# Kernel tuning notes

Hardware: AMD Instinct MI355X
Metric: run time of the kernel (lower is better)

The kernel has to match this reference:

```python
import jax, jax.numpy as jnp
import numpy as np

B, N, CIN, H, E = 1, 20000, 128, 128, 320000


def setup_inputs() -> dict:
    key = jax.random.key(0)
    ks = jax.random.split(key, 16)
    x = jax.random.normal(ks[0], (B, N, CIN), jnp.float32)
    edge_index = jax.random.randint(ks[1], (2, E), 0, N, dtype=jnp.int64)
    edge_weight = jax.random.uniform(ks[2], (E,), jnp.float32)
    h = jax.random.normal(ks[3], (B, N, H), jnp.float32)
    c = jax.random.normal(ks[4], (B, N, H), jnp.float32)
    # GCN stack params, gate order [i, f, c, o]; 2 layers each (K=2)
    Wx0 = jax.random.normal(ks[5], (4, CIN, H), jnp.float32) / np.float32(np.sqrt(CIN))
    bx0 = jnp.zeros((4, H), jnp.float32)
    Wx1 = jax.random.normal(ks[6], (4, H, H), jnp.float32) / np.float32(np.sqrt(H))
    bx1 = jnp.zeros((4, H), jnp.float32)
    Wh0 = jax.random.normal(ks[7], (4, H, H), jnp.float32) / np.float32(np.sqrt(H))
    bh0 = jnp.zeros((4, H), jnp.float32)
    Wh1 = jax.random.normal(ks[8], (4, H, H), jnp.float32) / np.float32(np.sqrt(H))
    bh1 = jnp.zeros((4, H), jnp.float32)
    wc = jax.random.normal(ks[9], (3, H), jnp.float32) * 0.1  # peephole [i, f, o]
    bg = jnp.zeros((4, H), jnp.float32)  # gate biases [i, f, c, o]
    return dict(x=x, edge_index=edge_index, edge_weight=edge_weight, h=h, c=c,
                Wx0=Wx0, bx0=bx0, Wx1=Wx1, bx1=bx1,
                Wh0=Wh0, bh0=bh0, Wh1=Wh1, bh1=bh1, wc=wc, bg=bg)


def reference(x, edge_index, edge_weight, h, c,
              Wx0, bx0, Wx1, bx1, Wh0, bh0, Wh1, bh1, wc, bg):
    n = x.shape[1]
    src, dst = edge_index[0], edge_index[1]
    loop = jnp.arange(n)
    src2 = jnp.concatenate([src, loop])
    dst2 = jnp.concatenate([dst, loop])
    w2 = jnp.concatenate([edge_weight, jnp.ones((n,), edge_weight.dtype)])
    deg = jax.ops.segment_sum(w2, dst2, num_segments=n)
    dis = jnp.where(deg > 0, jax.lax.rsqrt(jnp.maximum(deg, 1e-12)), 0.0)
    norm = dis[src2] * w2 * dis[dst2]  # sym GCN norm with self loops

    def prop(t):  # t: [..., N, F] -> D^-1/2 (A+I) D^-1/2 t
        lead = t.shape[:-2]
        tf = t.reshape((-1,) + t.shape[-2:])
        m = tf[:, src2, :] * norm[None, :, None]
        agg = jax.vmap(lambda mm: jax.ops.segment_sum(mm, dst2, num_segments=n))(m)
        return agg.reshape(lead + agg.shape[-2:])

    def gcn4(t, W0, b0, W1, b1):  # 2-layer GCN, 4 gates at once
        a = prop(t)  # shared first aggregation: [B,N,F]
        h0 = jax.nn.relu(jnp.einsum('bnc,gch->gbnh', a, W0) + b0[:, None, None, :])
        a1 = prop(h0)  # [4,B,N,H]
        return jnp.einsum('gbnh,ghk->gbnk', a1, W1) + b1[:, None, None, :]

    G = gcn4(x, Wx0, bx0, Wx1, bx1) + gcn4(h, Wh0, bh0, Wh1, bh1)  # [4,B,N,H]
    I = jax.nn.sigmoid(G[0] + wc[0] * c + bg[0])
    F = jax.nn.sigmoid(G[1] + wc[1] * c + bg[1])
    T = jnp.tanh(G[2] + bg[2])
    Cn = F * c + I * T
    O = jax.nn.sigmoid(G[3] + wc[2] * Cn + bg[3])
    Hn = O * jnp.tanh(Cn)
    return (Hn, Cn)
```

## Files before the change

kernel.cpp:

```cpp
#include <hip/hip_runtime.h>
#include <hip/hip_bf16.h>
#include <stdint.h>

#define NN    20000
#define NP    20096
#define EE    320000
#define CH    128
#define GC    512
#define NHtot 2560000

typedef short bf16x8 __attribute__((ext_vector_type(8)));
typedef float f32x4  __attribute__((ext_vector_type(4)));

__device__ __forceinline__ float bf2f(unsigned short u) {
    union { unsigned int i; float f; } c; c.i = ((unsigned int)u) << 16; return c.f;
}
__device__ __forceinline__ unsigned short f2bf(float f) {
    __hip_bfloat16 b = __float2bfloat16(f);
    union { __hip_bfloat16 b; unsigned short u; } c; c.b = b; return c.u;
}
__device__ __forceinline__ void unpack8(uint4 v, float* f) {
    f[0] = bf2f((unsigned short)(v.x & 0xffff)); f[1] = bf2f((unsigned short)(v.x >> 16));
    f[2] = bf2f((unsigned short)(v.y & 0xffff)); f[3] = bf2f((unsigned short)(v.y >> 16));
    f[4] = bf2f((unsigned short)(v.z & 0xffff)); f[5] = bf2f((unsigned short)(v.z >> 16));
    f[6] = bf2f((unsigned short)(v.w & 0xffff)); f[7] = bf2f((unsigned short)(v.w >> 16));
}
__device__ __forceinline__ void unpack4(uint2 v, float* f) {
    f[0] = bf2f((unsigned short)(v.x & 0xffff)); f[1] = bf2f((unsigned short)(v.x >> 16));
    f[2] = bf2f((unsigned short)(v.y & 0xffff)); f[3] = bf2f((unsigned short)(v.y >> 16));
}
__device__ __forceinline__ uint2 pack4(const float* f) {
    uint2 v;
    v.x = (unsigned int)f2bf(f[0]) | ((unsigned int)f2bf(f[1]) << 16);
    v.y = (unsigned int)f2bf(f[2]) | ((unsigned int)f2bf(f[3]) << 16);
    return v;
}

__global__ void k_count(const int* __restrict__ ei, int* __restrict__ cnt) {
    int e = blockIdx.x * 256 + threadIdx.x;
    if (e >= EE) return;
    atomicAdd(&cnt[ei[EE + e]], 1);
}

__global__ void k_scan1(const int* __restrict__ cnt, int* __restrict__ rowoff,
                        int* __restrict__ bsum) {
    __shared__ int wsum[4];
    int i = blockIdx.x * 256 + threadIdx.x;
    int self = (i < NN) ? cnt[i] : 0;
    int lane = threadIdx.x & 63, wid = threadIdx.x >> 6;
    int v = self;
    #pragma unroll
    for (int off = 1; off < 64; off <<= 1) {
        int u = __shfl_up(v, off);
        if (lane >= off) v += u;
    }
    if (lane == 63) wsum[wid] = v;
    __syncthreads();
    int wof = 0;
    for (int k = 0; k < wid; ++k) wof += wsum[k];
    if (i < NN) rowoff[i] = wof + v - self;
    if (threadIdx.x == 255) bsum[blockIdx.x] = wof + v;
}

__global__ void k_scan2(int* __restrict__ bsum) {
    int lane = threadIdx.x;
    int base = 0;
    for (int start = 0; start < 80; start += 64) {
        int i = start + lane;
        int self = (i < 80) ? bsum[i] : 0;
        int v = self;
        #pragma unroll
        for (int off = 1; off < 64; off <<= 1) {
            int u = __shfl_up(v, off);
            if (lane >= off) v += u;
        }
        if (i < 80) bsum[i] = base + v - self;
        base += __shfl(v, 63);
    }
}

__global__ void k_scan3(int* __restrict__ rowoff, const int* __restrict__ bsum,
                        int* __restrict__ cur) {
    int i = blockIdx.x * 256 + threadIdx.x;
    if (i < NN) {
        int v = rowoff[i] + bsum[i >> 8];
        rowoff[i] = v; cur[i] = v;
    }
    if (i == NN) rowoff[NN] = EE;
}

__global__ void k_scatter(const int* __restrict__ ei, const float* __restrict__ ew,
                          int* __restrict__ cur,
                          int* __restrict__ csrs, float* __restrict__ csrw) {
    int e = blockIdx.x * 256 + threadIdx.x;
    if (e >= EE) return;
    int s = ei[e], d = ei[EE + e];
    int p = atomicAdd(&cur[d], 1);
    csrs[p] = s; csrw[p] = ew[e];
}

__global__ void k_deg(const int* __restrict__ rowoff, const float* __restrict__ csrw,
                      float* __restrict__ dis) {
    int i = blockIdx.x * 256 + threadIdx.x;
    if (i >= NN) return;
    float s = 1.0f;
    int e1 = rowoff[i + 1];
    for (int e = rowoff[i]; e < e1; ++e) s += csrw[e];
    dis[i] = rsqrtf(fmaxf(s, 1e-12f));
}

__global__ void k_castxh(const float* __restrict__ x, const float* __restrict__ h,
                         const float* __restrict__ dis, unsigned short* __restrict__ xhb) {
    int idx = blockIdx.x * 256 + threadIdx.x;
    int n = idx >> 5, c4 = idx & 31;
    float dn = dis[n];
    float4 xv = *(const float4*)(x + (size_t)n * CH + c4 * 4);
    float4 hv = *(const float4*)(h + (size_t)n * CH + c4 * 4);
    float fx[4] = { dn * xv.x, dn * xv.y, dn * xv.z, dn * xv.w };
    float fh[4] = { dn * hv.x, dn * hv.y, dn * hv.z, dn * hv.w };
    *(uint2*)(xhb + (size_t)n * 256 + c4 * 4)       = pack4(fx);
    *(uint2*)(xhb + (size_t)n * 256 + 128 + c4 * 4) = pack4(fh);
}

__global__ __launch_bounds__(256) void k_prop256(
        const unsigned short* __restrict__ tab, unsigned short* __restrict__ o,
        const int* __restrict__ rowoff, const int* __restrict__ csrs,
        const float* __restrict__ csrw, const float* __restrict__ dis) {
    int w = blockIdx.x * 4 + (threadIdx.x >> 6);
    int lane = threadIdx.x & 63;
    const uint2* T2 = (const uint2*)tab;
    float acc[4], va[4], vb[4], vc[4], vd[4];
    uint2 v = T2[(size_t)w * 64 + lane];
    unpack4(v, va);
    #pragma unroll
    for (int j = 0; j < 4; ++j) acc[j] = va[j];
    int e = rowoff[w], e1 = rowoff[w + 1];
    for (; e + 4 <= e1; e += 4) {
        int   s0 = csrs[e],   s1 = csrs[e+1], s2 = csrs[e+2], s3 = csrs[e+3];
        float n0 = csrw[e],   n1 = csrw[e+1], n2 = csrw[e+2], n3 = csrw[e+3];
        uint2 u0 = T2[(size_t)s0 * 64 + lane];
        uint2 u1 = T2[(size_t)s1 * 64 + lane];
        uint2 u2 = T2[(size_t)s2 * 64 + lane];
        uint2 u3 = T2[(size_t)s3 * 64 + lane];
        unpack4(u0, va); unpack4(u1, vb); unpack4(u2, vc); unpack4(u3, vd);
        #pragma unroll
        for (int j = 0; j < 4; ++j)
            acc[j] += n0 * va[j] + n1 * vb[j] + n2 * vc[j] + n3 * vd[j];
    }
    for (; e < e1; ++e) {
        int s = csrs[e]; float nw = csrw[e];
        v = T2[(size_t)s * 64 + lane];
        unpack4(v, va);
        #pragma unroll
        for (int j = 0; j < 4; ++j) acc[j] += nw * va[j];
    }
    float dw = dis[w];
    #pragma unroll
    for (int j = 0; j < 4; ++j) acc[j] *= dw;
    ((uint2*)o)[(size_t)w * 64 + lane] = pack4(acc);
}

__global__ void k_prepw(const float* __restrict__ W0, const float* __restrict__ W1,
                        const float* __restrict__ W2, const float* __restrict__ W3,
                        unsigned short* __restrict__ T0, unsigned short* __restrict__ T1,
                        unsigned short* __restrict__ T2, unsigned short* __restrict__ T3) {
    const float* W; unsigned short* T;
    switch (blockIdx.z) {
        case 0:  W = W0; T = T0; break;
        case 1:  W = W1; T = T1; break;
        case 2:  W = W2; T = T2; break;
        default: W = W3; T = T3; break;
    }
    int g = blockIdx.y;
    int n = blockIdx.x * 2 + (threadIdx.x >> 7);
    int k = threadIdx.x & 127;
    T[((size_t)g * 128 + n) * 128 + k] = f2bf(W[((size_t)g * 128 + k) * 128 + n]);
}

__global__ void k_prepb(const float* __restrict__ bx1, const float* __restrict__ bh1,
                        const float* __restrict__ bg, float* __restrict__ btot) {
    int f = blockIdx.x * 256 + threadIdx.x;
    if (f < GC) btot[f] = bx1[f] + bh1[f] + bg[f];
}

#define SWZ(r, c8) (((r) << 4) + ((c8) ^ ((r) & 15)))

__global__ __launch_bounds__(256) void k_gemm1(
        const unsigned short* __restrict__ A,
        const unsigned short* __restrict__ Wtx, const unsigned short* __restrict__ Wth,
        const float* __restrict__ bx0, const float* __restrict__ bh0,
        unsigned short* __restrict__ outx, unsigned short* __restrict__ outh) {
    __shared__ uint4 As[2048];
    __shared__ uint4 Bs[2048];
    const int side = blockIdx.z;
    const int aoff = side * 128;
    const unsigned short* Wt = side ? Wth : Wtx;
    const float* bias        = side ? bh0 : bx0;
    unsigned short* out      = side ? outh : outx;

    const int    g    = blockIdx.y;
    const size_t row0 = (size_t)blockIdx.x * 128;
    const int    t    = threadIdx.x;

    #pragma unroll
    for (int p = 0; p < 8; ++p) {
        int id = t + 256 * p, r = id >> 4, c8 = id & 15;
        As[SWZ(r, c8)] = *(const uint4*)(A + (row0 + r) * 256 + aoff + c8 * 8);
    }
    const unsigned short* Wg = Wt + (size_t)g * 16384;
    #pragma unroll
    for (int p = 0; p < 8; ++p) {
        int id = t + 256 * p, r = id >> 4, c8 = id & 15;
        Bs[SWZ(r, c8)] = *(const uint4*)(Wg + r * CH + c8 * 8);
    }
    __syncthreads();

    const int wid = t >> 6, l = t & 63;
    const int m0 = (wid >> 1) * 64, n0 = (wid & 1) * 64;
    const int lm = l & 15, q = l >> 4;
    f32x4 acc[4][4];
    #pragma unroll
    for (int i = 0; i < 4; ++i)
        #pragma unroll
        for (int j = 0; j < 4; ++j) { acc[i][j][0]=0.f; acc[i][j][1]=0.f; acc[i][j][2]=0.f; acc[i][j][3]=0.f; }

    #pragma unroll
    for (int kc = 0; kc < 4; ++kc) {
        int c8 = kc * 4 + q;
        bf16x8 a[4], b[4];
        #pragma unroll
        for (int i = 0; i < 4; ++i) { int r = m0 + i * 16 + lm; a[i] = *(const bf16x8*)&As[SWZ(r, c8)]; }
        #pragma unroll
        for (int j = 0; j < 4; ++j) { int r = n0 + j * 16 + lm; b[j] = *(const bf16x8*)&Bs[SWZ(r, c8)]; }
        #pragma unroll
        for (int i = 0; i < 4; ++i)
            #pragma unroll
            for (int j = 0; j < 4; ++j)
                acc[i][j] = __builtin_amdgcn_mfma_f32_16x16x32_bf16(a[i], b[j], acc[i][j], 0, 0, 0);
    }

    #pragma unroll
    for (int j = 0; j < 4; ++j) {
        float bb = bias[g * CH + n0 + j * 16 + lm];
        #pragma unroll
        for (int i = 0; i < 4; ++i)
            #pragma unroll
            for (int r = 0; r < 4; ++r) {
                int rowl = m0 + i * 16 + q * 4 + r;
                int col  = n0 + j * 16 + lm;
                out[(row0 + rowl) * GC + g * CH + col] = f2bf(fmaxf(acc[i][j][r] + bb, 0.f));
            }
    }
}

__global__ __launch_bounds__(256) void k_gemm2(
        const unsigned short* __restrict__ A1, const unsigned short* __restrict__ A2,
        const unsigned short* __restrict__ Wt1, const unsigned short* __restrict__ Wt2,
        const float* __restrict__ dis, unsigned short* __restrict__ outS) {
    __shared__ uint4 As[2048];
    __shared__ uint4 Bs[2048];
    const int    g    = blockIdx.y;
    const size_t row0 = (size_t)blockIdx.x * 128;
    const int    t    = threadIdx.x;
    const int wid = t >> 6, l = t & 63;
    const int m0 = (wid >> 1) * 64, n0 = (wid & 1) * 64;
    const int lm = l & 15, q = l >> 4;
    f32x4 acc[4][4];
    #pragma unroll
    for (int i = 0; i < 4; ++i)
        #pragma unroll
        for (int j = 0; j < 4; ++j) { acc[i][j][0]=0.f; acc[i][j][1]=0.f; acc[i][j][2]=0.f; acc[i][j][3]=0.f; }

    for (int side = 0; side < 2; ++side) {
        if (side) __syncthreads();
        const unsigned short* Ap = side ? A2 : A1;
        const unsigned short* Wg = (side ? Wt2 : Wt1) + (size_t)g * 16384;
        #pragma unroll
        for (int p = 0; p < 8; ++p) {
            int id = t + 256 * p, r = id >> 4, c8 = id & 15;
            As[SWZ(r, c8)] = *(const uint4*)(Ap + (row0 + r) * GC + g * CH + c8 * 8);
        }
        #pragma unroll
        for (int p = 0; p < 8; ++p) {
            int id = t + 256 * p, r = id >> 4, c8 = id & 15;
            Bs[SWZ(r, c8)] = *(const uint4*)(Wg + r * CH + c8 * 8);
        }
        __syncthreads();
        #pragma unroll
        for (int kc = 0; kc < 4; ++kc) {
            int c8 = kc * 4 + q;
            bf16x8 a[4], b[4];
            #pragma unroll
            for (int i = 0; i < 4; ++i) { int r = m0 + i * 16 + lm; a[i] = *(const bf16x8*)&As[SWZ(r, c8)]; }
            #pragma unroll
            for (int j = 0; j < 4; ++j) { int r = n0 + j * 16 + lm; b[j] = *(const bf16x8*)&Bs[SWZ(r, c8)]; }
            #pragma unroll
            for (int i = 0; i < 4; ++i)
                #pragma unroll
                for (int j = 0; j < 4; ++j)
                    acc[i][j] = __builtin_amdgcn_mfma_f32_16x16x32_bf16(a[i], b[j], acc[i][j], 0, 0, 0);
        }
    }

    #pragma unroll
    for (int j = 0; j < 4; ++j)
        #pragma unroll
        for (int i = 0; i < 4; ++i)
            #pragma unroll
            for (int r = 0; r < 4; ++r) {
                int rowl = m0 + i * 16 + q * 4 + r;
                int col  = n0 + j * 16 + lm;
                float dr = dis[row0 + rowl];
                outS[(row0 + rowl) * GC + g * CH + col] = f2bf(dr * acc[i][j][r]);
            }
}

#define GIDX(f) ((f) + ((f) >> 5))
__global__ __launch_bounds__(256) void k_prop512g(
        const unsigned short* __restrict__ Sb, float* __restrict__ out,
        const int* __restrict__ rowoff, const int* __restrict__ csrs,
        const float* __restrict__ csrw, const float* __restrict__ dis,
        const float* __restrict__ c, const float* __restrict__ btot,
        const float* __restrict__ wc) {
    __shared__ float gbuf[4][528];
    int wid  = threadIdx.x >> 6, lane = threadIdx.x & 63;
    int w    = blockIdx.x * 4 + wid;
    const uint4* S4 = (const uint4*)Sb;
    float acc[8], va[8], vb[8], vc4[8], vd[8];
    uint4 v = S4[(size_t)w * 64 + lane];
    unpack8(v, acc);
    int e = rowoff[w], e1 = rowoff[w + 1];
    for (; e + 4 <= e1; e += 4) {
        int   s0 = csrs[e],   s1 = csrs[e+1], s2 = csrs[e+2], s3 = csrs[e+3];
        float n0 = csrw[e],   n1 = csrw[e+1], n2 = csrw[e+2], n3 = csrw[e+3];
        uint4 u0 = S4[(size_t)s0 * 64 + lane];
        uint4 u1 = S4[(size_t)s1 * 64 + lane];
        uint4 u2 = S4[(size_t)s2 * 64 + lane];
        uint4 u3 = S4[(size_t)s3 * 64 + lane];
        unpack8(u0, va); unpack8(u1, vb); unpack8(u2, vc4); unpack8(u3, vd);
        #pragma unroll
        for (int j = 0; j < 8; ++j)
            acc[j] += n0 * va[j] + n1 * vb[j] + n2 * vc4[j] + n3 * vd[j];
    }
    for (; e < e1; ++e) {
        int s = csrs[e]; float nw = csrw[e];
        v = S4[(size_t)s * 64 + lane];
        unpack8(v, va);
        #pragma unroll
        for (int j = 0; j < 8; ++j) acc[j] += nw * va[j];
    }
    float dw = dis[w];
    #pragma unroll
    for (int j = 0; j < 8; ++j) {
        int f = lane * 8 + j;
        gbuf[wid][GIDX(f)] = dw * acc[j];
    }
    __syncthreads();
    const float* gb = gbuf[wid];
    #pragma unroll
    for (int t2 = 0; t2 < 2; ++t2) {
        int hh = lane + 64 * t2;
        float g0 = gb[GIDX(hh)]       + btot[hh];
        float g1 = gb[GIDX(128 + hh)] + btot[128 + hh];
        float g2 = gb[GIDX(256 + hh)] + btot[256 + hh];
        float g3 = gb[GIDX(384 + hh)] + btot[384 + hh];
        float cv = c[(size_t)w * CH + hh];
        float I  = 1.f / (1.f + expf(-(g0 + wc[hh]       * cv)));
        float F  = 1.f / (1.f + expf(-(g1 + wc[128 + hh] * cv)));
        float T  = tanhf(g2);
        float Cn = F * cv + I * T;
        float O  = 1.f / (1.f + expf(-(g3 + wc[256 + hh] * Cn)));
        out[(size_t)w * CH + hh]         = O * tanhf(Cn);
        out[NHtot + (size_t)w * CH + hh] = Cn;
    }
}

extern "C" void kernel_launch(void* const* d_in, const int* in_sizes, int n_in,
                              void* d_out, int out_size, void* d_ws, size_t ws_size,
                              hipStream_t stream) {
    (void)in_sizes; (void)n_in; (void)out_size; (void)ws_size;
    const float* x   = (const float*)d_in[0];
    const int*   ei  = (const int*)d_in[1];
    const float* ew  = (const float*)d_in[2];
    const float* h   = (const float*)d_in[3];
    const float* c   = (const float*)d_in[4];
    const float* Wx0 = (const float*)d_in[5];
    const float* bx0 = (const float*)d_in[6];
    const float* Wx1 = (const float*)d_in[7];
    const float* bx1 = (const float*)d_in[8];
    const float* Wh0 = (const float*)d_in[9];
    const float* bh0 = (const float*)d_in[10];
    const float* Wh1 = (const float*)d_in[11];
    const float* bh1 = (const float*)d_in[12];
    const float* wc  = (const float*)d_in[13];
    const float* bg  = (const float*)d_in[14];
    float* out = (float*)d_out;

    float* wsf  = (float*)d_ws;
    float* dis  = wsf;
    int*   cnt  = (int*)(wsf + 20480);
    int*   row  = (int*)(wsf + 40960);
    int*   cur  = (int*)(wsf + 61696);
    int*   bsum = (int*)(wsf + 82176);
    float* btot = wsf + 82432;
    int*   csrs = (int*)(wsf + 82944);
    float* csrw = wsf + 402944;
    unsigned short* Wt0x = (unsigned short*)(wsf + 722944);
    unsigned short* Wt0h = (unsigned short*)(wsf + 755712);
    unsigned short* Wt1x = (unsigned short*)(wsf + 788480);
    unsigned short* Wt1h = (unsigned short*)(wsf + 821248);
    unsigned short* xhb  = (unsigned short*)(wsf + 854016);
    unsigned short* axh  = (unsigned short*)(wsf + 3426304);
    unsigned short* h0x  = (unsigned short*)(wsf + 5998592);
    unsigned short* h0h  = (unsigned short*)(wsf + 11143168);
    unsigned short* Sb   = (unsigned short*)(wsf + 16287744);

    hipMemsetAsync(cnt, 0, 20480 * sizeof(int), stream);

    k_count  <<<EE / 256, 256, 0, stream>>>(ei, cnt);
    k_scan1  <<<80, 256, 0, stream>>>(cnt, row, bsum);
    k_scan2  <<<1, 64, 0, stream>>>(bsum);
    k_scan3  <<<80, 256, 0, stream>>>(row, bsum, cur);
    k_scatter<<<EE / 256, 256, 0, stream>>>(ei, ew, cur, csrs, csrw);
    k_deg    <<<(NN + 255) / 256, 256, 0, stream>>>(row, csrw, dis);

    dim3 pw(64, 4, 4);
    k_prepw  <<<pw, 256, 0, stream>>>(Wx0, Wh0, Wx1, Wh1, Wt0x, Wt0h, Wt1x, Wt1h);
    k_prepb  <<<2, 256, 0, stream>>>(bx1, bh1, bg, btot);
    k_castxh <<<NN * 32 / 256, 256, 0, stream>>>(x, h, dis, xhb);

    k_prop256<<<NN / 4, 256, 0, stream>>>(xhb, axh, row, csrs, csrw, dis);

    dim3 g1(NP / 128, 4, 2);
    k_gemm1<<<g1, 256, 0, stream>>>(axh, Wt0x, Wt0h, bx0, bh0, h0x, h0h);
    dim3 g2(NP / 128, 4);
    k_gemm2<<<g2, 256, 0, stream>>>(h0x, h0h, Wt1x, Wt1h, dis, Sb);

    k_prop512g<<<NN / 4, 256, 0, stream>>>(Sb, out, row, csrs, csrw, dis, c, btot, wc);
}
```

Before: 265.9 us.

## Fuse two GCN GEMMs via LDS, merge degree and cast, unroll gathers

```diff
diff --git a/kernel.cpp b/kernel.cpp
--- a/kernel.cpp
+++ b/kernel.cpp
@@ -99,27 +99,47 @@
     csrs[p] = s; csrw[p] = ew[e];
 }
 
-__global__ void k_deg(const int* __restrict__ rowoff, const float* __restrict__ csrw,
-                      float* __restrict__ dis) {
-    int i = blockIdx.x * 256 + threadIdx.x;
-    if (i >= NN) return;
-    float s = 1.0f;
-    int e1 = rowoff[i + 1];
-    for (int e = rowoff[i]; e < e1; ++e) s += csrw[e];
-    dis[i] = rsqrtf(fmaxf(s, 1e-12f));
-}
-
-__global__ void k_castxh(const float* __restrict__ x, const float* __restrict__ h,
-                         const float* __restrict__ dis, unsigned short* __restrict__ xhb) {
-    int idx = blockIdx.x * 256 + threadIdx.x;
-    int n = idx >> 5, c4 = idx & 31;
-    float dn = dis[n];
-    float4 xv = *(const float4*)(x + (size_t)n * CH + c4 * 4);
-    float4 hv = *(const float4*)(h + (size_t)n * CH + c4 * 4);
-    float fx[4] = { dn * xv.x, dn * xv.y, dn * xv.z, dn * xv.w };
-    float fh[4] = { dn * hv.x, dn * hv.y, dn * hv.z, dn * hv.w };
-    *(uint2*)(xhb + (size_t)n * 256 + c4 * 4)       = pack4(fx);
-    *(uint2*)(xhb + (size_t)n * 256 + 128 + c4 * 4) = pack4(fh);
+__global__ __launch_bounds__(256) void k_degcast(
+        const float* __restrict__ x, const float* __restrict__ h,
+        const int* __restrict__ rowoff, const float* __restrict__ csrw,
+        float* __restrict__ dis, unsigned short* __restrict__ xhb) {
+    int wid = threadIdx.x >> 6, lane = threadIdx.x & 63;
+    int w = blockIdx.x * 4 + wid;
+    int e0 = rowoff[w], e1 = rowoff[w + 1];
+    float s = 0.f;
+    for (int e = e0 + lane; e < e1; e += 64) s += csrw[e];
+    #pragma unroll
+    for (int off = 32; off; off >>= 1) s += __shfl_xor(s, off);
+    float dn = rsqrtf(fmaxf(1.0f + s, 1e-12f));
+    if (lane == 0) dis[w] = dn;
+    const float* src = (lane < 32) ? x + (size_t)w * CH + lane * 4
+                                   : h + (size_t)w * CH + (lane - 32) * 4;
+    float4 v = *(const float4*)src;
+    float f[4] = { dn * v.x, dn * v.y, dn * v.z, dn * v.w };
+    *(uint2*)(xhb + (size_t)w * 256 + lane * 4) = pack4(f);
+}
+
+__global__ void k_prepw(const float* __restrict__ W0, const float* __restrict__ W1,
+                        const float* __restrict__ W2, const float* __restrict__ W3,
+                        unsigned short* __restrict__ T0, unsigned short* __restrict__ T1,
+                        unsigned short* __restrict__ T2, unsigned short* __restrict__ T3,
+                        const float* __restrict__ bx1, const float* __restrict__ bh1,
+                        const float* __restrict__ bg, float* __restrict__ btot) {
+    if (blockIdx.z == 0 && blockIdx.y == 0 && blockIdx.x < 2) {
+        int f = blockIdx.x * 256 + threadIdx.x;
+        btot[f] = bx1[f] + bh1[f] + bg[f];
+    }
+    const float* W; unsigned short* T;
+    switch (blockIdx.z) {
+        case 0:  W = W0; T = T0; break;
+        case 1:  W = W1; T = T1; break;
+        case 2:  W = W2; T = T2; break;
+        default: W = W3; T = T3; break;
+    }
+    int g = blockIdx.y;
+    int n = blockIdx.x * 2 + (threadIdx.x >> 7);
+    int k = threadIdx.x & 127;
+    T[((size_t)g * 128 + n) * 128 + k] = f2bf(W[((size_t)g * 128 + k) * 128 + n]);
 }
 
 __global__ __launch_bounds__(256) void k_prop256(
@@ -129,23 +149,31 @@
     int w = blockIdx.x * 4 + (threadIdx.x >> 6);
     int lane = threadIdx.x & 63;
     const uint2* T2 = (const uint2*)tab;
-    float acc[4], va[4], vb[4], vc[4], vd[4];
+    float acc[4], va[4];
     uint2 v = T2[(size_t)w * 64 + lane];
-    unpack4(v, va);
-    #pragma unroll
-    for (int j = 0; j < 4; ++j) acc[j] = va[j];
+    unpack4(v, acc);
     int e = rowoff[w], e1 = rowoff[w + 1];
-    for (; e + 4 <= e1; e += 4) {
+    for (; e + 8 <= e1; e += 8) {
         int   s0 = csrs[e],   s1 = csrs[e+1], s2 = csrs[e+2], s3 = csrs[e+3];
-        float n0 = csrw[e],   n1 = csrw[e+1], n2 = csrw[e+2], n3 = csrw[e+3];
+        int   s4 = csrs[e+4], s5 = csrs[e+5], s6 = csrs[e+6], s7 = csrs[e+7];
         uint2 u0 = T2[(size_t)s0 * 64 + lane];
         uint2 u1 = T2[(size_t)s1 * 64 + lane];
         uint2 u2 = T2[(size_t)s2 * 64 + lane];
         uint2 u3 = T2[(size_t)s3 * 64 + lane];
-        unpack4(u0, va); unpack4(u1, vb); unpack4(u2, vc); unpack4(u3, vd);
-        #pragma unroll
-        for (int j = 0; j < 4; ++j)
-            acc[j] += n0 * va[j] + n1 * vb[j] + n2 * vc[j] + n3 * vd[j];
+        uint2 u4 = T2[(size_t)s4 * 64 + lane];
+        uint2 u5 = T2[(size_t)s5 * 64 + lane];
+        uint2 u6 = T2[(size_t)s6 * 64 + lane];
+        uint2 u7 = T2[(size_t)s7 * 64 + lane];
+        float n0 = csrw[e],   n1 = csrw[e+1], n2 = csrw[e+2], n3 = csrw[e+3];
+        float n4 = csrw[e+4], n5 = csrw[e+5], n6 = csrw[e+6], n7 = csrw[e+7];
+        unpack4(u0, va); acc[0]+=n0*va[0]; acc[1]+=n0*va[1]; acc[2]+=n0*va[2]; acc[3]+=n0*va[3];
+        unpack4(u1, va); acc[0]+=n1*va[0]; acc[1]+=n1*va[1]; acc[2]+=n1*va[2]; acc[3]+=n1*va[3];
+        unpack4(u2, va); acc[0]+=n2*va[0]; acc[1]+=n2*va[1]; acc[2]+=n2*va[2]; acc[3]+=n2*va[3];
+        unpack4(u3, va); acc[0]+=n3*va[0]; acc[1]+=n3*va[1]; acc[2]+=n3*va[2]; acc[3]+=n3*va[3];
+        unpack4(u4, va); acc[0]+=n4*va[0]; acc[1]+=n4*va[1]; acc[2]+=n4*va[2]; acc[3]+=n4*va[3];
+        unpack4(u5, va); acc[0]+=n5*va[0]; acc[1]+=n5*va[1]; acc[2]+=n5*va[2]; acc[3]+=n5*va[3];
+        unpack4(u6, va); acc[0]+=n6*va[0]; acc[1]+=n6*va[1]; acc[2]+=n6*va[2]; acc[3]+=n6*va[3];
+        unpack4(u7, va); acc[0]+=n7*va[0]; acc[1]+=n7*va[1]; acc[2]+=n7*va[2]; acc[3]+=n7*va[3];
     }
     for (; e < e1; ++e) {
         int s = csrs[e]; float nw = csrw[e];
@@ -160,103 +188,14 @@
     ((uint2*)o)[(size_t)w * 64 + lane] = pack4(acc);
 }
 
-__global__ void k_prepw(const float* __restrict__ W0, const float* __restrict__ W1,
-                        const float* __restrict__ W2, const float* __restrict__ W3,
-                        unsigned short* __restrict__ T0, unsigned short* __restrict__ T1,
-                        unsigned short* __restrict__ T2, unsigned short* __restrict__ T3) {
-    const float* W; unsigned short* T;
-    switch (blockIdx.z) {
-        case 0:  W = W0; T = T0; break;
-        case 1:  W = W1; T = T1; break;
-        case 2:  W = W2; T = T2; break;
-        default: W = W3; T = T3; break;
-    }
-    int g = blockIdx.y;
-    int n = blockIdx.x * 2 + (threadIdx.x >> 7);
-    int k = threadIdx.x & 127;
-    T[((size_t)g * 128 + n) * 128 + k] = f2bf(W[((size_t)g * 128 + k) * 128 + n]);
-}
-
-__global__ void k_prepb(const float* __restrict__ bx1, const float* __restrict__ bh1,
-                        const float* __restrict__ bg, float* __restrict__ btot) {
-    int f = blockIdx.x * 256 + threadIdx.x;
-    if (f < GC) btot[f] = bx1[f] + bh1[f] + bg[f];
-}
-
 #define SWZ(r, c8) (((r) << 4) + ((c8) ^ ((r) & 15)))
 
-__global__ __launch_bounds__(256) void k_gemm1(
-        const unsigned short* __restrict__ A,
-        const unsigned short* __restrict__ Wtx, const unsigned short* __restrict__ Wth,
+__global__ __launch_bounds__(256) void k_gemmF(
+        const unsigned short* __restrict__ axh,
+        const unsigned short* __restrict__ Wt0x, const unsigned short* __restrict__ Wt0h,
+        const unsigned short* __restrict__ Wt1x, const unsigned short* __restrict__ Wt1h,
         const float* __restrict__ bx0, const float* __restrict__ bh0,
-        unsigned short* __restrict__ outx, unsigned short* __restrict__ outh) {
-    __shared__ uint4 As[2048];
-    __shared__ uint4 Bs[2048];
-    const int side = blockIdx.z;
-    const int aoff = side * 128;
-    const unsigned short* Wt = side ? Wth : Wtx;
-    const float* bias        = side ? bh0 : bx0;
-    unsigned short* out      = side ? outh : outx;
-
-    const int    g    = blockIdx.y;
-    const size_t row0 = (size_t)blockIdx.x * 128;
-    const int    t    = threadIdx.x;
-
-    #pragma unroll
-    for (int p = 0; p < 8; ++p) {
-        int id = t + 256 * p, r = id >> 4, c8 = id & 15;
-        As[SWZ(r, c8)] = *(const uint4*)(A + (row0 + r) * 256 + aoff + c8 * 8);
-    }
-    const unsigned short* Wg = Wt + (size_t)g * 16384;
-    #pragma unroll
-    for (int p = 0; p < 8; ++p) {
-        int id = t + 256 * p, r = id >> 4, c8 = id & 15;
-        Bs[SWZ(r, c8)] = *(const uint4*)(Wg + r * CH + c8 * 8);
-    }
-    __syncthreads();
-
-    const int wid = t >> 6, l = t & 63;
-    const int m0 = (wid >> 1) * 64, n0 = (wid & 1) * 64;
-    const int lm = l & 15, q = l >> 4;
-    f32x4 acc[4][4];
-    #pragma unroll
-    for (int i = 0; i < 4; ++i)
-        #pragma unroll
-        for (int j = 0; j < 4; ++j) { acc[i][j][0]=0.f; acc[i][j][1]=0.f; acc[i][j][2]=0.f; acc[i][j][3]=0.f; }
-
-    #pragma unroll
-    for (int kc = 0; kc < 4; ++kc) {
-        int c8 = kc * 4 + q;
-        bf16x8 a[4], b[4];
-        #pragma unroll
-        for (int i = 0; i < 4; ++i) { int r = m0 + i * 16 + lm; a[i] = *(const bf16x8*)&As[SWZ(r, c8)]; }
-        #pragma unroll
-        for (int j = 0; j < 4; ++j) { int r = n0 + j * 16 + lm; b[j] = *(const bf16x8*)&Bs[SWZ(r, c8)]; }
-        #pragma unroll
-        for (int i = 0; i < 4; ++i)
-            #pragma unroll
-            for (int j = 0; j < 4; ++j)
-                acc[i][j] = __builtin_amdgcn_mfma_f32_16x16x32_bf16(a[i], b[j], acc[i][j], 0, 0, 0);
-    }
-
-    #pragma unroll
-    for (int j = 0; j < 4; ++j) {
-        float bb = bias[g * CH + n0 + j * 16 + lm];
-        #pragma unroll
-        for (int i = 0; i < 4; ++i)
-            #pragma unroll
-            for (int r = 0; r < 4; ++r) {
-                int rowl = m0 + i * 16 + q * 4 + r;
-                int col  = n0 + j * 16 + lm;
-                out[(row0 + rowl) * GC + g * CH + col] = f2bf(fmaxf(acc[i][j][r] + bb, 0.f));
-            }
-    }
-}
-
-__global__ __launch_bounds__(256) void k_gemm2(
-        const unsigned short* __restrict__ A1, const unsigned short* __restrict__ A2,
-        const unsigned short* __restrict__ Wt1, const unsigned short* __restrict__ Wt2,
-        const float* __restrict__ dis, unsigned short* __restrict__ outS) {
+        const float* __restrict__ dis, unsigned short* __restrict__ Sb) {
     __shared__ uint4 As[2048];
     __shared__ uint4 Bs[2048];
     const int    g    = blockIdx.y;
@@ -265,27 +204,32 @@
     const int wid = t >> 6, l = t & 63;
     const int m0 = (wid >> 1) * 64, n0 = (wid & 1) * 64;
     const int lm = l & 15, q = l >> 4;
-    f32x4 acc[4][4];
+    f32x4 sacc[4][4];
     #pragma unroll
     for (int i = 0; i < 4; ++i)
         #pragma unroll
-        for (int j = 0; j < 4; ++j) { acc[i][j][0]=0.f; acc[i][j][1]=0.f; acc[i][j][2]=0.f; acc[i][j][3]=0.f; }
+        for (int j = 0; j < 4; ++j) { sacc[i][j][0]=0.f; sacc[i][j][1]=0.f; sacc[i][j][2]=0.f; sacc[i][j][3]=0.f; }
 
     for (int side = 0; side < 2; ++side) {
         if (side) __syncthreads();
-        const unsigned short* Ap = side ? A2 : A1;
-        const unsigned short* Wg = (side ? Wt2 : Wt1) + (size_t)g * 16384;
         #pragma unroll
         for (int p = 0; p < 8; ++p) {
             int id = t + 256 * p, r = id >> 4, c8 = id & 15;
-            As[SWZ(r, c8)] = *(const uint4*)(Ap + (row0 + r) * GC + g * CH + c8 * 8);
-        }
+            As[SWZ(r, c8)] = *(const uint4*)(axh + (row0 + r) * 256 + side * 128 + c8 * 8);
+        }
+        const unsigned short* W0 = (side ? Wt0h : Wt0x) + (size_t)g * 16384;
         #pragma unroll
         for (int p = 0; p < 8; ++p) {
             int id = t + 256 * p, r = id >> 4, c8 = id & 15;
-            Bs[SWZ(r, c8)] = *(const uint4*)(Wg + r * CH + c8 * 8);
+            Bs[SWZ(r, c8)] = *(const uint4*)(W0 + r * CH + c8 * 8);
         }
         __syncthreads();
+
+        f32x4 hacc[4][4];
+        #pragma unroll
+        for (int i = 0; i < 4; ++i)
+            #pragma unroll
+            for (int j = 0; j < 4; ++j) { hacc[i][j][0]=0.f; hacc[i][j][1]=0.f; hacc[i][j][2]=0.f; hacc[i][j][3]=0.f; }
         #pragma unroll
         for (int kc = 0; kc < 4; ++kc) {
             int c8 = kc * 4 + q;
@@ -298,7 +242,45 @@
             for (int i = 0; i < 4; ++i)
                 #pragma unroll
                 for (int j = 0; j < 4; ++j)
-                    acc[i][j] = __builtin_amdgcn_mfma_f32_16x16x32_bf16(a[i], b[j], acc[i][j], 0, 0, 0);
+                    hacc[i][j] = __builtin_amdgcn_mfma_f32_16x16x32_bf16(a[i], b[j], hacc[i][j], 0, 0, 0);
+        }
+        __syncthreads();
+
+        const float* b0 = side ? bh0 : bx0;
+        unsigned short* Hs = (unsigned short*)As;
+        #pragma unroll
+        for (int j = 0; j < 4; ++j) {
+            int col = n0 + j * 16 + lm;
+            float bb = b0[g * CH + col];
+            #pragma unroll
+            for (int i = 0; i < 4; ++i)
+                #pragma unroll
+                for (int r = 0; r < 4; ++r) {
+                    int row = m0 + i * 16 + q * 4 + r;
+                    Hs[SWZ(row, col >> 3) * 8 + (col & 7)] = f2bf(fmaxf(hacc[i][j][r] + bb, 0.f));
+                }
+        }
+        const unsigned short* W1 = (side ? Wt1h : Wt1x) + (size_t)g * 16384;
+        #pragma unroll
+        for (int p = 0; p < 8; ++p) {
+            int id = t + 256 * p, r = id >> 4, c8 = id & 15;
+            Bs[SWZ(r, c8)] = *(const uint4*)(W1 + r * CH + c8 * 8);
+        }
+        __syncthreads();
+
+        #pragma unroll
+        for (int kc = 0; kc < 4; ++kc) {
+            int c8 = kc * 4 + q;
+            bf16x8 a[4], b[4];
+            #pragma unroll
+            for (int i = 0; i < 4; ++i) { int r = m0 + i * 16 + lm; a[i] = *(const bf16x8*)&As[SWZ(r, c8)]; }
+            #pragma unroll
+            for (int j = 0; j < 4; ++j) { int r = n0 + j * 16 + lm; b[j] = *(const bf16x8*)&Bs[SWZ(r, c8)]; }
+            #pragma unroll
+            for (int i = 0; i < 4; ++i)
+                #pragma unroll
+                for (int j = 0; j < 4; ++j)
+                    sacc[i][j] = __builtin_amdgcn_mfma_f32_16x16x32_bf16(a[i], b[j], sacc[i][j], 0, 0, 0);
         }
     }
 
@@ -311,7 +293,7 @@
                 int rowl = m0 + i * 16 + q * 4 + r;
                 int col  = n0 + j * 16 + lm;
                 float dr = dis[row0 + rowl];
-                outS[(row0 + rowl) * GC + g * CH + col] = f2bf(dr * acc[i][j][r]);
+                Sb[(row0 + rowl) * GC + g * CH + col] = f2bf(dr * sacc[i][j][r]);
             }
 }
 
@@ -326,21 +308,47 @@
     int wid  = threadIdx.x >> 6, lane = threadIdx.x & 63;
     int w    = blockIdx.x * 4 + wid;
     const uint4* S4 = (const uint4*)Sb;
-    float acc[8], va[8], vb[8], vc4[8], vd[8];
+    float acc[8], va[8];
     uint4 v = S4[(size_t)w * 64 + lane];
     unpack8(v, acc);
     int e = rowoff[w], e1 = rowoff[w + 1];
-    for (; e + 4 <= e1; e += 4) {
+    for (; e + 8 <= e1; e += 8) {
         int   s0 = csrs[e],   s1 = csrs[e+1], s2 = csrs[e+2], s3 = csrs[e+3];
-        float n0 = csrw[e],   n1 = csrw[e+1], n2 = csrw[e+2], n3 = csrw[e+3];
+        int   s4 = csrs[e+4], s5 = csrs[e+5], s6 = csrs[e+6], s7 = csrs[e+7];
         uint4 u0 = S4[(size_t)s0 * 64 + lane];
         uint4 u1 = S4[(size_t)s1 * 64 + lane];
         uint4 u2 = S4[(size_t)s2 * 64 + lane];
         uint4 u3 = S4[(size_t)s3 * 64 + lane];
-        unpack8(u0, va); unpack8(u1, vb); unpack8(u2, vc4); unpack8(u3, vd);
-        #pragma unroll
-        for (int j = 0; j < 8; ++j)
-            acc[j] += n0 * va[j] + n1 * vb[j] + n2 * vc4[j] + n3 * vd[j];
+        uint4 u4 = S4[(size_t)s4 * 64 + lane];
+        uint4 u5 = S4[(size_t)s5 * 64 + lane];
+        uint4 u6 = S4[(size_t)s6 * 64 + lane];
+        uint4 u7 = S4[(size_t)s7 * 64 + lane];
+        float n0 = csrw[e],   n1 = csrw[e+1], n2 = csrw[e+2], n3 = csrw[e+3];
+        float n4 = csrw[e+4], n5 = csrw[e+5], n6 = csrw[e+6], n7 = csrw[e+7];
+        unpack8(u0, va);
+        #pragma unroll
+        for (int j = 0; j < 8; ++j) acc[j] += n0 * va[j];
+        unpack8(u1, va);
+        #pragma unroll
+        for (int j = 0; j < 8; ++j) acc[j] += n1 * va[j];
+        unpack8(u2, va);
+        #pragma unroll
+        for (int j = 0; j < 8; ++j) acc[j] += n2 * va[j];
+        unpack8(u3, va);
+        #pragma unroll
+        for (int j = 0; j < 8; ++j) acc[j] += n3 * va[j];
+        unpack8(u4, va);
+        #pragma unroll
+        for (int j = 0; j < 8; ++j) acc[j] += n4 * va[j];
+        unpack8(u5, va);
+        #pragma unroll
+        for (int j = 0; j < 8; ++j) acc[j] += n5 * va[j];
+        unpack8(u6, va);
+        #pragma unroll
+        for (int j = 0; j < 8; ++j) acc[j] += n6 * va[j];
+        unpack8(u7, va);
+        #pragma unroll
+        for (int j = 0; j < 8; ++j) acc[j] += n7 * va[j];
     }
     for (; e < e1; ++e) {
         int s = csrs[e]; float nw = csrw[e];
@@ -411,8 +419,6 @@
     unsigned short* Wt1h = (unsigned short*)(wsf + 821248);
     unsigned short* xhb  = (unsigned short*)(wsf + 854016);
     unsigned short* axh  = (unsigned short*)(wsf + 3426304);
-    unsigned short* h0x  = (unsigned short*)(wsf + 5998592);
-    unsigned short* h0h  = (unsigned short*)(wsf + 11143168);
     unsigned short* Sb   = (unsigned short*)(wsf + 16287744);
 
     hipMemsetAsync(cnt, 0, 20480 * sizeof(int), stream);
@@ -422,19 +428,16 @@
     k_scan2  <<<1, 64, 0, stream>>>(bsum);
     k_scan3  <<<80, 256, 0, stream>>>(row, bsum, cur);
     k_scatter<<<EE / 256, 256, 0, stream>>>(ei, ew, cur, csrs, csrw);
-    k_deg    <<<(NN + 255) / 256, 256, 0, stream>>>(row, csrw, dis);
 
     dim3 pw(64, 4, 4);
-    k_prepw  <<<pw, 256, 0, stream>>>(Wx0, Wh0, Wx1, Wh1, Wt0x, Wt0h, Wt1x, Wt1h);
-    k_prepb  <<<2, 256, 0, stream>>>(bx1, bh1, bg, btot);
-    k_castxh <<<NN * 32 / 256, 256, 0, stream>>>(x, h, dis, xhb);
+    k_prepw  <<<pw, 256, 0, stream>>>(Wx0, Wh0, Wx1, Wh1, Wt0x, Wt0h, Wt1x, Wt1h,
+                                      bx1, bh1, bg, btot);
+    k_degcast<<<NN / 4, 256, 0, stream>>>(x, h, row, csrw, dis, xhb);
 
     k_prop256<<<NN / 4, 256, 0, stream>>>(xhb, axh, row, csrs, csrw, dis);
 
-    dim3 g1(NP / 128, 4, 2);
-    k_gemm1<<<g1, 256, 0, stream>>>(axh, Wt0x, Wt0h, bx0, bh0, h0x, h0h);
-    dim3 g2(NP / 128, 4);
-    k_gemm2<<<g2, 256, 0, stream>>>(h0x, h0h, Wt1x, Wt1h, dis, Sb);
+    dim3 gf(NP / 128, 4);
+    k_gemmF<<<gf, 256, 0, stream>>>(axh, Wt0x, Wt0h, Wt1x, Wt1h, bx0, bh0, dis, Sb);
 
     k_prop512g<<<NN / 4, 256, 0, stream>>>(Sb, out, row, csrs, csrw, dis, c, btot, wc);
 }
```

Measured after the change: 288.8 us. 8.6% more time.
